# Kernel optimization log

Hardware: AMD Instinct MI355X
Metric: run time of the kernel (lower is better)

## Reference

```python
import jax, jax.numpy as jnp
import numpy as np

EPS = 1e-6

def _layernorm(x, g, b):
    mu = jnp.mean(x, axis=-1, keepdims=True)
    var = jnp.mean(jnp.square(x - mu), axis=-1, keepdims=True)
    return (x - mu) * jax.lax.rsqrt(var + EPS) * g + b

def _mhsa(xq, xk, xv, mask, Wq, bq, Wk, bk, Wv, bv, Wo, bo, num_heads):
    B, Nq, D = xq.shape
    Nk = xk.shape[1]
    dh = D // num_heads
    # project then split heads: [B, N, D] -> [B, H, N, dh]
    def split(x, W, b, N):
        return (x @ W + b).reshape(B, N, num_heads, dh).transpose(0, 2, 1, 3)
    q = split(xq, Wq, bq, Nq)
    k = split(xk, Wk, bk, Nk)
    v = split(xv, Wv, bv, Nk)
    scores = jnp.einsum('bhnd,bhmd->bhnm', q, k) / jnp.sqrt(jnp.float32(dh))
    if mask is not None:
        scores = scores + mask * (-1e9)
    w = jax.nn.softmax(scores, axis=-1)
    out = jnp.einsum('bhnm,bhmd->bhnd', w, v)          # [B,H,Nq,dh]
    out = out.transpose(0, 2, 1, 3).reshape(B, Nq, D)  # concat heads
    return out @ Wo + bo

def setup_inputs() -> dict:
    B, N, D, FF = 2, 2048, 512, 2048
    key = jax.random.key(0)
    ks = jax.random.split(key, 32)
    std = 0.02
    p = {}
    p['inputs'] = jax.random.normal(ks[0], (B, N, D), jnp.float32)
    p['enc_output'] = jax.random.normal(ks[1], (B, N, D), jnp.float32)
    # causal look-ahead mask: 1 where masked (future positions)
    p['look_ahead_mask'] = jnp.triu(jnp.ones((N, N), jnp.float32), k=1)[None, None]
    p['padding_mask'] = jnp.zeros((B, 1, 1, N), jnp.float32)
    i = 2
    for pre in ('q1', 'k1', 'v1', 'o1', 'q2', 'k2', 'v2', 'o2'):
        p[pre + '_w'] = jax.random.normal(ks[i], (D, D), jnp.float32) * std; i += 1
        p[pre + '_b'] = jnp.zeros((D,), jnp.float32)
    p['f1_w'] = jax.random.normal(ks[i], (D, FF), jnp.float32) * std; i += 1
    p['f1_b'] = jnp.zeros((FF,), jnp.float32)
    p['f2_w'] = jax.random.normal(ks[i], (FF, D), jnp.float32) * std; i += 1
    p['f2_b'] = jnp.zeros((D,), jnp.float32)
    for ln in ('ln1', 'ln2', 'ln3'):
        p[ln + '_g'] = jnp.ones((D,), jnp.float32)
        p[ln + '_b'] = jnp.zeros((D,), jnp.float32)
    p['training'] = 0
    return p

def reference(inputs, enc_output, look_ahead_mask, padding_mask,
              q1_w, q1_b, k1_w, k1_b, v1_w, v1_b, o1_w, o1_b,
              q2_w, q2_b, k2_w, k2_b, v2_w, v2_b, o2_w, o2_b,
              f1_w, f1_b, f2_w, f2_b,
              ln1_g, ln1_b, ln2_g, ln2_b, ln3_g, ln3_b,
              training):
    H = 8
    # self-attention (q=k=v=inputs), causal mask; dropout inactive (eval)
    attn1 = _mhsa(inputs, inputs, inputs, look_ahead_mask,
                  q1_w, q1_b, k1_w, k1_b, v1_w, v1_b, o1_w, o1_b, H)
    out1 = _layernorm(inputs + attn1, ln1_g, ln1_b)
    # cross attention: NOTE original arg order -> q=enc, k=enc, v=out1
    attn2 = _mhsa(enc_output, enc_output, out1, padding_mask,
                  q2_w, q2_b, k2_w, k2_b, v2_w, v2_b, o2_w, o2_b, H)
    out2 = _layernorm(out1 + attn2, ln2_g, ln2_b)
    ffn = jax.nn.relu(out2 @ f1_w + f1_b) @ f2_w + f2_b
    return _layernorm(out2 + ffn, ln3_g, ln3_b)
```

## Files before the change

kernel.cpp:

```cpp
#include <hip/hip_runtime.h>

typedef __attribute__((ext_vector_type(8))) _Float16 half8;
typedef __attribute__((ext_vector_type(4))) _Float16 half4;
typedef __attribute__((ext_vector_type(2))) _Float16 half2_t;
typedef __attribute__((ext_vector_type(2))) __fp16 fp16x2;
typedef __attribute__((ext_vector_type(4))) float f32x4;

#define AS1 __attribute__((address_space(1)))
#define AS3 __attribute__((address_space(3)))

constexpr int SEQ = 2048, DM = 512, FFD = 2048, NH = 8, DH = 64;
constexpr int M = 2 * SEQ;
constexpr float QSCALE = 0.125f * 1.4426950408889634f;

__global__ __launch_bounds__(256)
void preproc(const float* __restrict__ q1_w, const float* __restrict__ k1_w,
             const float* __restrict__ v1_w, const float* __restrict__ o1_w,
             const float* __restrict__ q2_w, const float* __restrict__ k2_w,
             const float* __restrict__ v2_w, const float* __restrict__ o2_w,
             const float* __restrict__ f1_w, const float* __restrict__ f2_w,
             _Float16* __restrict__ qk1t, _Float16* __restrict__ v1t,
             _Float16* __restrict__ o1t, _Float16* __restrict__ qk2t,
             _Float16* __restrict__ v2t, _Float16* __restrict__ o2t,
             _Float16* __restrict__ f1t, _Float16* __restrict__ f2t,
             const float* __restrict__ q1_b, const float* __restrict__ k1_b,
             const float* __restrict__ q2_b, const float* __restrict__ k2_b,
             float* __restrict__ qk1b, float* __restrict__ qk2b,
             const float* __restrict__ inp, const float* __restrict__ enc,
             _Float16* __restrict__ xh, _Float16* __restrict__ eh) {
    __shared__ _Float16 tile[64 * 65];
    const int j = blockIdx.x, tid = threadIdx.x;
    if (j < 1024) {
        const float* src; _Float16* dst; int K, N, n0, k0;
        if (j < 512) {
            int w8 = j >> 6, t = j & 63;
            K = 512; N = 512; n0 = (t & 7) * 64; k0 = (t >> 3) * 64;
            switch (w8) {
                case 0: src = q1_w; dst = qk1t; break;
                case 1: src = k1_w; dst = qk1t + 512 * 512; break;
                case 2: src = v1_w; dst = v1t; break;
                case 3: src = o1_w; dst = o1t; break;
                case 4: src = q2_w; dst = qk2t; break;
                case 5: src = k2_w; dst = qk2t + 512 * 512; break;
                case 6: src = v2_w; dst = v2t; break;
                default: src = o2_w; dst = o2t; break;
            }
        } else if (j < 768) {
            int t = j - 512; K = 512; N = 2048;
            n0 = (t % 32) * 64; k0 = (t / 32) * 64; src = f1_w; dst = f1t;
        } else {
            int t = j - 768; K = 2048; N = 512;
            n0 = (t % 8) * 64; k0 = (t / 8) * 64; src = f2_w; dst = f2t;
        }
        int c = tid & 63, r4 = tid >> 6;
        for (int i = 0; i < 16; i++) {
            int r = r4 * 16 + i;
            tile[r * 65 + c] = (_Float16)src[(size_t)(k0 + r) * N + n0 + c];
        }
        __syncthreads();
        for (int i = 0; i < 16; i++) {
            int r = r4 * 16 + i;
            dst[(size_t)(n0 + r) * K + k0 + c] = tile[c * 65 + r];
        }
    } else if (j == 1024) {
        for (int i = tid; i < 512; i += 256) { qk1b[i] = q1_b[i]; qk1b[512 + i] = k1_b[i]; }
    } else if (j == 1025) {
        for (int i = tid; i < 512; i += 256) { qk2b[i] = q2_b[i]; qk2b[512 + i] = k2_b[i]; }
    } else {
        int k = j - 1026;
        const float* s = (k < 1024) ? inp : enc;
        _Float16* d = (k < 1024) ? xh : eh;
        size_t base = (size_t)(k & 1023) * 2048 + tid * 8;
        f32x4 a = *(const f32x4*)(s + base);
        f32x4 b2 = *(const f32x4*)(s + base + 4);
        half8 h;
        h[0] = (_Float16)a[0]; h[1] = (_Float16)a[1];
        h[2] = (_Float16)a[2]; h[3] = (_Float16)a[3];
        h[4] = (_Float16)b2[0]; h[5] = (_Float16)b2[1];
        h[6] = (_Float16)b2[2]; h[7] = (_Float16)b2[3];
        *(half8*)(d + base) = h;
    }
}

__global__ __launch_bounds__(256)
void qkv_gemm(const _Float16* __restrict__ xh, const _Float16* __restrict__ eh,
              const _Float16* __restrict__ qk1t, const _Float16* __restrict__ qk2t,
              const float* __restrict__ qk1b, const float* __restrict__ qk2b,
              _Float16* __restrict__ Qh1, _Float16* __restrict__ Kh1,
              _Float16* __restrict__ Qh2, _Float16* __restrict__ Kh2,
              const _Float16* __restrict__ v1t, const float* __restrict__ v1b,
              _Float16* __restrict__ V1T) {
    __shared__ _Float16 smem[192 * 64];
    const int tid = threadIdx.x;
    const int wid = tid >> 6, lid = tid & 63;
    const int wr = (wid & 1) * 64;
    const int wc = (wid >> 1) * 32;
    const int mi = lid & 15, qd = lid >> 4;
    const int jb = blockIdx.x;
    const _Float16 *Ap, *Bp;
    const float* bias;
    int m0, n0, epi, job = 0;
    if (jb < 1024) {
        epi = 4; job = jb >> 9;
        int L = jb & 511;
        int by = L % 32, bx = L / 32;
        m0 = by * 128; n0 = bx * 64;
        Ap = (job ? eh : xh) + (size_t)m0 * 512;
        Bp = (job ? qk2t : qk1t) + (size_t)n0 * 512;
        bias = job ? qk2b : qk1b;
    } else {
        epi = 3;
        int t = jb - 1024;
        int by = t & 3, bx = t >> 2;
        m0 = by * 128; n0 = bx * 64;
        Ap = v1t + (size_t)m0 * 512;
        Bp = xh + (size_t)n0 * 512;
        bias = v1b;
    }
    const int lrow = lid >> 3;
    const int gblk = (lid & 7) ^ ((lid >> 3) & 7);
    auto stage = [&](int kt) {
        #pragma unroll
        for (int l = 0; l < 4; l++) {
            int c = l * 4 + wid;
            int row = c * 8 + lrow;
            __builtin_amdgcn_global_load_lds(
                (const AS1 unsigned int*)(Ap + (size_t)row * 512 + kt * 64 + gblk * 8),
                (AS3 unsigned int*)&smem[c * 512], 16, 0, 0);
        }
        #pragma unroll
        for (int l = 0; l < 2; l++) {
            int c = l * 4 + wid;
            int row = c * 8 + lrow;
            __builtin_amdgcn_global_load_lds(
                (const AS1 unsigned int*)(Bp + (size_t)row * 512 + kt * 64 + gblk * 8),
                (AS3 unsigned int*)&smem[128 * 64 + c * 512], 16, 0, 0);
        }
    };
    f32x4 acc[4][2] = {};
    stage(0);
    __builtin_amdgcn_s_waitcnt(0x0F70);
    __syncthreads();
    for (int t = 0; t < 8; t++) {
        #pragma unroll
        for (int h = 0; h < 2; h++) {
            const int sA = ((4 * h + qd) ^ (mi & 7)) * 8;
            half8 af[4], bfr[2];
            #pragma unroll
            for (int i = 0; i < 4; i++)
                af[i] = *(const half8*)&smem[(wr + i * 16 + mi) * 64 + sA];
            #pragma unroll
            for (int j = 0; j < 2; j++)
                bfr[j] = *(const half8*)&smem[(128 + wc + j * 16 + mi) * 64 + sA];
            #pragma unroll
            for (int i = 0; i < 4; i++)
                #pragma unroll
                for (int j = 0; j < 2; j++)
                    acc[i][j] = __builtin_amdgcn_mfma_f32_16x16x32_f16(af[i], bfr[j], acc[i][j], 0, 0, 0);
        }
        if (t + 1 < 8) {
            __syncthreads();
            stage(t + 1);
            __builtin_amdgcn_s_waitcnt(0x0F70);
            __syncthreads();
        }
    }
    #pragma unroll
    for (int i = 0; i < 4; i++) {
        #pragma unroll
        for (int j = 0; j < 2; j++) {
            #pragma unroll
            for (int r = 0; r < 4; r++) {
                int row = m0 + wr + i * 16 + qd * 4 + r;
                int col = n0 + wc + j * 16 + mi;
                float v = acc[i][j][r];
                if (epi == 4) {
                    v += bias[col];
                    int hh2 = (col >> 6) & 7, d = col & 63;
                    int bb = row >> 11, nn = row & 2047;
                    size_t idx = (((size_t)bb * 8 + hh2) * SEQ + nn) * 64 + d;
                    if (col < 512) (job ? Qh2 : Qh1)[idx] = (_Float16)(v * QSCALE);
                    else           (job ? Kh2 : Kh1)[idx] = (_Float16)v;
                } else {
                    v += bias[row];
                    V1T[(size_t)row * 4096 + col] = (_Float16)v;
                }
            }
        }
    }
}

template<int BM, int BN, int WM, int WN, bool RELU, int EPI, int SPLIT>
__global__ __launch_bounds__(256)
void gemm_tn(const _Float16* __restrict__ A, const _Float16* __restrict__ Bt,
             const float* __restrict__ bias,
             float* __restrict__ outF, _Float16* __restrict__ outH,
             int Mtot, int N, int K) {
    constexpr int ROWS = BM + BN;
    __shared__ _Float16 smem[ROWS * 64];
    constexpr int AF = WM / 16, BF = WN / 16;
    constexpr int WROW = BM / WM;
    const int tid = threadIdx.x;
    const int wid = tid >> 6, lid = tid & 63;
    const int wr = (wid % WROW) * WM;
    const int wc = (wid / WROW) * WN;
    const int mi = lid & 15, qd = lid >> 4;
    const int gx = gridDim.x, gy = gridDim.y;
    const int L = blockIdx.y * gx + blockIdx.x;
    const int by = L % gy, bx = L / gy;
    const int m0 = by * BM, n0 = bx * BN;
    const int Kc = K / SPLIT;
    const int kbase = (SPLIT > 1) ? blockIdx.z * Kc : 0;
    const _Float16* Ap = A + (size_t)m0 * K + kbase;
    const _Float16* Bp = Bt + (size_t)n0 * K + kbase;
    const int lrow = lid >> 3;
    const int gblk = (lid & 7) ^ ((lid >> 3) & 7);
    auto stage = [&](int kt) {
        #pragma unroll
        for (int l = 0; l < BM / 32; l++) {
            int c = l * 4 + wid;
            int row = c * 8 + lrow;
            __builtin_amdgcn_global_load_lds(
                (const AS1 unsigned int*)(Ap + (size_t)row * K + kt * 64 + gblk * 8),
                (AS3 unsigned int*)&smem[c * 512], 16, 0, 0);
        }
        #pragma unroll
        for (int l = 0; l < BN / 32; l++) {
            int c = l * 4 + wid;
            int row = c * 8 + lrow;
            __builtin_amdgcn_global_load_lds(
                (const AS1 unsigned int*)(Bp + (size_t)row * K + kt * 64 + gblk * 8),
                (AS3 unsigned int*)&smem[BM * 64 + c * 512], 16, 0, 0);
        }
    };
    f32x4 acc[AF][BF] = {};
    const int NIT = Kc / 64;
    stage(0);
    __builtin_amdgcn_s_waitcnt(0x0F70);
    __syncthreads();
    for (int t = 0; t < NIT; t++) {
        #pragma unroll
        for (int h = 0; h < 2; h++) {
            const int sA = ((4 * h + qd) ^ (mi & 7)) * 8;
            half8 af[AF], bfr[BF];
            #pragma unroll
            for (int i = 0; i < AF; i++)
                af[i] = *(const half8*)&smem[(wr + i * 16 + mi) * 64 + sA];
            #pragma unroll
            for (int j = 0; j < BF; j++)
                bfr[j] = *(const half8*)&smem[(BM + wc + j * 16 + mi) * 64 + sA];
            #pragma unroll
            for (int i = 0; i < AF; i++)
                #pragma unroll
                for (int j = 0; j < BF; j++)
                    acc[i][j] = __builtin_amdgcn_mfma_f32_16x16x32_f16(af[i], bfr[j], acc[i][j], 0, 0, 0);
        }
        if (t + 1 < NIT) {
            __syncthreads();
            stage(t + 1);
            __builtin_amdgcn_s_waitcnt(0x0F70);
            __syncthreads();
        }
    }
    float* oF = outF;
    if (SPLIT > 1 && outF) oF = outF + (size_t)blockIdx.z * Mtot * N;
    _Float16* oH = outH;
    if (EPI == 5) oH = outH + (size_t)blockIdx.z * Mtot * N;
    const bool doBias = bias && (SPLIT == 1 || blockIdx.z == 0);
    #pragma unroll
    for (int i = 0; i < AF; i++) {
        #pragma unroll
        for (int j = 0; j < BF; j++) {
            #pragma unroll
            for (int r = 0; r < 4; r++) {
                int row = m0 + wr + i * 16 + qd * 4 + r;
                int col = n0 + wc + j * 16 + mi;
                float v = acc[i][j][r];
                if (EPI == 3) {
                    v += bias[row];
                    outH[(size_t)row * N + col] = (_Float16)v;
                } else if (EPI == 5) {
                    if (doBias) v += bias[col];
                    oH[(size_t)row * N + col] = (_Float16)v;
                } else {
                    if (doBias) v += bias[col];
                    if (RELU) v = fmaxf(v, 0.f);
                    size_t off = (size_t)row * N + col;
                    if (oF) oF[off] = v;
                    if (outH) outH[off] = (_Float16)v;
                }
            }
        }
    }
}

template<bool CAUSAL>
__global__ __launch_bounds__(512)
void attn_mono(const _Float16* __restrict__ Qh, const _Float16* __restrict__ Kh,
               const _Float16* __restrict__ VT, int ldv,
               _Float16* __restrict__ O) {
    const int x = blockIdx.x, bh = blockIdx.y;
    int qt;
    if (CAUSAL) {
        int half = x >> 1;
        int pick = (x & 1) ^ ((bh >> 3) & 1);
        qt = pick ? half : 31 - half;
    } else {
        qt = x;
    }
    const int nt = CAUSAL ? (qt + 1) : 32;
    const int np = (nt + 1) >> 1;
    __shared__ _Float16 Qs[64 * 64];
    __shared__ _Float16 Ps[2][64 * 64];
    __shared__ _Float16 Ks[2][64 * 64];
    __shared__ _Float16 Vs[2][64 * 64];
    __shared__ float Lsh[64];
    const int tid = threadIdx.x, w = tid >> 6, lane = tid & 63;
    const int w4 = w & 3, st = w >> 2;
    const int mi = lane & 15, qd = lane >> 4;
    const int qbase = qt * 64;
    const int b = bh >> 3, h = bh & 7;
    const _Float16* Qp = Qh + ((size_t)bh * SEQ + qbase) * 64;
    const _Float16* Kp = Kh + (size_t)bh * SEQ * 64;
    const _Float16* Vp = VT + (size_t)(h * 64) * ldv + (size_t)b * SEQ;
    const int lrow = lane >> 3;
    const int gblk = (lane & 7) ^ ((lane >> 3) & 7);
    const int f0 = (qd ^ (mi & 7)) * 8;
    const int f1 = ((qd + 4) ^ (mi & 7)) * 8;

    {
        int r0 = tid >> 3, blk = tid & 7;
        int sw = (blk ^ (r0 & 7)) * 8;
        half8 q0 = *(const half8*)(Qp + r0 * 64 + blk * 8);
        *(half8*)&Qs[r0 * 64 + sw] = q0;
    }
    __syncthreads();
    half8 qb0 = *(half8*)&Qs[(w4 * 16 + mi) * 64 + f0];
    half8 qb1 = *(half8*)&Qs[(w4 * 16 + mi) * 64 + f1];
    f32x4 oacc[4] = {};
    float lacc = 0.f;
    _Float16* Pst = Ps[st];

    for (int i = 0; i < np; i++) {
        const int t = 2 * i + st;
        const bool act = t < nt;
        __syncthreads();
        if (act) {
            #pragma unroll
            for (int l = 0; l < 2; l++) {
                int cc = l * 4 + w4;
                int row = cc * 8 + lrow;
                __builtin_amdgcn_global_load_lds(
                    (const AS1 unsigned int*)(Kp + ((size_t)(t * 64 + row)) * 64 + gblk * 8),
                    (AS3 unsigned int*)&Ks[st][cc * 512], 16, 0, 0);
                __builtin_amdgcn_global_load_lds(
                    (const AS1 unsigned int*)(Vp + (size_t)row * ldv + t * 64 + gblk * 8),
                    (AS3 unsigned int*)&Vs[st][cc * 512], 16, 0, 0);
            }
        }
        __builtin_amdgcn_s_waitcnt(0x0F70);
        __syncthreads();
        if (!act) continue;
        const _Float16* ksb = Ks[st];
        const _Float16* vsb = Vs[st];
        f32x4 s[4];
        #pragma unroll
        for (int j = 0; j < 4; j++) {
            half8 ka0 = *(const half8*)&ksb[(j * 16 + mi) * 64 + f0];
            half8 ka1 = *(const half8*)&ksb[(j * 16 + mi) * 64 + f1];
            f32x4 a = {};
            a = __builtin_amdgcn_mfma_f32_16x16x32_f16(ka0, qb0, a, 0, 0, 0);
            a = __builtin_amdgcn_mfma_f32_16x16x32_f16(ka1, qb1, a, 0, 0, 0);
            s[j] = a;
        }
        if (CAUSAL && t == qt) {
            int qg = qbase + w4 * 16 + mi;
            #pragma unroll
            for (int j = 0; j < 4; j++)
                #pragma unroll
                for (int r = 0; r < 4; r++) {
                    int key = t * 64 + j * 16 + qd * 4 + r;
                    if (key > qg) s[j][r] = -1e30f;
                }
        }
        #pragma unroll
        for (int j = 0; j < 4; j++)
            #pragma unroll
            for (int r = 0; r < 4; r++) {
                float pv = __builtin_amdgcn_exp2f(s[j][r]);
                s[j][r] = pv;
                lacc += pv;
            }
        #pragma unroll
        for (int j = 0; j < 4; j++) {
            fp16x2 lo = __builtin_amdgcn_cvt_pkrtz(s[j][0], s[j][1]);
            fp16x2 hi = __builtin_amdgcn_cvt_pkrtz(s[j][2], s[j][3]);
            half2_t lo2 = __builtin_bit_cast(half2_t, lo);
            half2_t hi2 = __builtin_bit_cast(half2_t, hi);
            half4 pq;
            pq[0] = lo2[0]; pq[1] = lo2[1]; pq[2] = hi2[0]; pq[3] = hi2[1];
            int blkp = (2 * j + (qd >> 1)) ^ (mi & 7);
            *(half4*)&Pst[(w4 * 16 + mi) * 64 + blkp * 8 + (qd & 1) * 4] = pq;
        }
        half8 pa0 = *(half8*)&Pst[(w4 * 16 + mi) * 64 + f0];
        half8 pa1 = *(half8*)&Pst[(w4 * 16 + mi) * 64 + f1];
        #pragma unroll
        for (int j = 0; j < 4; j++) {
            half8 vb0 = *(const half8*)&vsb[(j * 16 + mi) * 64 + f0];
            half8 vb1 = *(const half8*)&vsb[(j * 16 + mi) * 64 + f1];
            oacc[j] = __builtin_amdgcn_mfma_f32_16x16x32_f16(pa0, vb0, oacc[j], 0, 0, 0);
            oacc[j] = __builtin_amdgcn_mfma_f32_16x16x32_f16(pa1, vb1, oacc[j], 0, 0, 0);
        }
    }
    __syncthreads();
    if (st == 1) {
        float* obuf = (float*)Ks;
        float* lbuf = (float*)Vs;
        int base = (w4 * 64 + lane) * 16;
        #pragma unroll
        for (int j = 0; j < 4; j++)
            #pragma unroll
            for (int r = 0; r < 4; r++)
                obuf[base + j * 4 + r] = oacc[j][r];
        lbuf[w4 * 64 + lane] = lacc;
    }
    __syncthreads();
    if (st == 0) {
        const float* obuf = (const float*)Ks;
        const float* lbuf = (const float*)Vs;
        int base = (w4 * 64 + lane) * 16;
        #pragma unroll
        for (int j = 0; j < 4; j++)
            #pragma unroll
            for (int r = 0; r < 4; r++)
                oacc[j][r] += obuf[base + j * 4 + r];
        lacc += lbuf[w4 * 64 + lane];
        lacc += __shfl_xor(lacc, 16, 64);
        lacc += __shfl_xor(lacc, 32, 64);
        if (qd == 0) Lsh[w4 * 16 + mi] = lacc;
    }
    __syncthreads();
    if (st == 0) {
        #pragma unroll
        for (int r = 0; r < 4; r++) {
            float rl = 1.f / Lsh[w4 * 16 + qd * 4 + r];
            int qrow = qbase + w4 * 16 + qd * 4 + r;
            size_t obase = ((size_t)(b * SEQ + qrow)) * 512 + h * 64;
            #pragma unroll
            for (int j = 0; j < 4; j++)
                O[obase + j * 16 + mi] = (_Float16)(oacc[j][r] * rl);
        }
    }
}

template<typename RT>
__global__ __launch_bounds__(256)
void add_ln(const RT* __restrict__ res, const _Float16* __restrict__ y,
            size_t pstride, int nparts,
            const float* __restrict__ g, const float* __restrict__ bb,
            float* __restrict__ outF, _Float16* __restrict__ outH) {
    int row = blockIdx.x;
    int tid = threadIdx.x;
    size_t base = (size_t)row * 512;
    float x0 = (float)res[base + tid];
    float x1 = (float)res[base + tid + 256];
    for (int s = 0; s < nparts; s++) {
        x0 += (float)y[s * pstride + base + tid];
        x1 += (float)y[s * pstride + base + tid + 256];
    }
    float s = x0 + x1, sq = x0 * x0 + x1 * x1;
    #pragma unroll
    for (int off = 32; off > 0; off >>= 1) {
        s += __shfl_xor(s, off, 64);
        sq += __shfl_xor(sq, off, 64);
    }
    __shared__ float ls[4], lq[4];
    int w = tid >> 6;
    if ((tid & 63) == 0) { ls[w] = s; lq[w] = sq; }
    __syncthreads();
    s = ls[0] + ls[1] + ls[2] + ls[3];
    sq = lq[0] + lq[1] + lq[2] + lq[3];
    float mu = s * (1.f / 512.f);
    float var = sq * (1.f / 512.f) - mu * mu;
    float rs = rsqrtf(var + 1e-6f);
    float o0 = (x0 - mu) * rs * g[tid] + bb[tid];
    float o1 = (x1 - mu) * rs * g[tid + 256] + bb[tid + 256];
    if (outF) { outF[base + tid] = o0; outF[base + tid + 256] = o1; }
    if (outH) { outH[base + tid] = (_Float16)o0; outH[base + tid + 256] = (_Float16)o1; }
}

extern "C" void kernel_launch(void* const* d_in, const int* in_sizes, int n_in,
                              void* d_out, int out_size, void* d_ws, size_t ws_size,
                              hipStream_t stream) {
    (void)in_sizes; (void)n_in; (void)out_size; (void)ws_size;
    const float* inp  = (const float*)d_in[0];
    const float* enc  = (const float*)d_in[1];
    const float* q1_w = (const float*)d_in[4];
    const float* q1_b = (const float*)d_in[5];
    const float* k1_w = (const float*)d_in[6];
    const float* k1_b = (const float*)d_in[7];
    const float* v1_w = (const float*)d_in[8];
    const float* v1_b = (const float*)d_in[9];
    const float* o1_w = (const float*)d_in[10];
    const float* o1_b = (const float*)d_in[11];
    const float* q2_w = (const float*)d_in[12];
    const float* q2_b = (const float*)d_in[13];
    const float* k2_w = (const float*)d_in[14];
    const float* k2_b = (const float*)d_in[15];
    const float* v2_w = (const float*)d_in[16];
    const float* v2_b = (const float*)d_in[17];
    const float* o2_w = (const float*)d_in[18];
    const float* o2_b = (const float*)d_in[19];
    const float* f1_w = (const float*)d_in[20];
    const float* f1_b = (const float*)d_in[21];
    const float* f2_w = (const float*)d_in[22];
    const float* f2_b = (const float*)d_in[23];
    const float* ln1_g = (const float*)d_in[24];
    const float* ln1_b = (const float*)d_in[25];
    const float* ln2_g = (const float*)d_in[26];
    const float* ln2_b = (const float*)d_in[27];
    const float* ln3_g = (const float*)d_in[28];
    const float* ln3_b = (const float*)d_in[29];

    char* p = (char*)d_ws;
    auto alloc = [&](size_t bytes) { char* r = p; p += (bytes + 255) & ~(size_t)255; return (void*)r; };
    _Float16* xh    = (_Float16*)alloc((size_t)M * DM * 2);
    _Float16* eh    = (_Float16*)alloc((size_t)M * DM * 2);
    _Float16* qk1t  = (_Float16*)alloc((size_t)1024 * DM * 2);
    _Float16* v1t   = (_Float16*)alloc((size_t)DM * DM * 2);
    _Float16* o1t   = (_Float16*)alloc((size_t)DM * DM * 2);
    _Float16* qk2t  = (_Float16*)alloc((size_t)1024 * DM * 2);
    _Float16* v2t   = (_Float16*)alloc((size_t)DM * DM * 2);
    _Float16* o2t   = (_Float16*)alloc((size_t)DM * DM * 2);
    _Float16* f1t   = (_Float16*)alloc((size_t)FFD * DM * 2);
    _Float16* f2t   = (_Float16*)alloc((size_t)DM * FFD * 2);
    float* qk1b     = (float*)alloc(1024 * 4);
    float* qk2b     = (float*)alloc(1024 * 4);
    _Float16* Qh1   = (_Float16*)alloc((size_t)M * DM * 2);
    _Float16* Kh1   = (_Float16*)alloc((size_t)M * DM * 2);
    _Float16* Qh2   = (_Float16*)alloc((size_t)M * DM * 2);
    _Float16* Kh2   = (_Float16*)alloc((size_t)M * DM * 2);
    _Float16* V1T   = (_Float16*)alloc((size_t)DM * M * 2);
    _Float16* V2T   = (_Float16*)alloc((size_t)DM * M * 2);
    _Float16* Ah    = (_Float16*)alloc((size_t)M * DM * 2);
    _Float16* Ph    = (_Float16*)alloc((size_t)2 * M * DM * 2);
    _Float16* out1h = (_Float16*)alloc((size_t)M * DM * 2);
    _Float16* out2h = (_Float16*)alloc((size_t)M * DM * 2);
    _Float16* hh    = (_Float16*)alloc((size_t)M * FFD * 2);
    const size_t PS = (size_t)M * DM;

    dim3 t256(256), t512(512);
    preproc<<<dim3(1026 + 2048), t256, 0, stream>>>(
        q1_w, k1_w, v1_w, o1_w, q2_w, k2_w, v2_w, o2_w, f1_w, f2_w,
        qk1t, v1t, o1t, qk2t, v2t, o2t, f1t, f2t,
        q1_b, k1_b, q2_b, k2_b, qk1b, qk2b, inp, enc, xh, eh);

    qkv_gemm<<<dim3(1280), t256, 0, stream>>>(
        xh, eh, qk1t, qk2t, qk1b, qk2b, Qh1, Kh1, Qh2, Kh2, v1t, v1_b, V1T);

    attn_mono<true><<<dim3(32, 16), t512, 0, stream>>>(Qh1, Kh1, V1T, M, Ah);
    gemm_tn<64, 64, 32, 32, false, 5, 2><<<dim3(8, 64, 2), t256, 0, stream>>>(
        Ah, o1t, o1_b, nullptr, Ph, M, 512, 512);
    add_ln<float><<<dim3(M), t256, 0, stream>>>(inp, Ph, PS, 2, ln1_g, ln1_b, nullptr, out1h);

    gemm_tn<64, 64, 32, 32, false, 3, 1><<<dim3(64, 8), t256, 0, stream>>>(
        v2t, out1h, v2_b, nullptr, V2T, 512, M, 512);
    attn_mono<false><<<dim3(32, 16), t512, 0, stream>>>(Qh2, Kh2, V2T, M, Ah);
    gemm_tn<64, 64, 32, 32, false, 5, 2><<<dim3(8, 64, 2), t256, 0, stream>>>(
        Ah, o2t, o2_b, nullptr, Ph, M, 512, 512);
    add_ln<_Float16><<<dim3(M), t256, 0, stream>>>(out1h, Ph, PS, 2, ln2_g, ln2_b, nullptr, out2h);

    gemm_tn<128, 64, 64, 32, true, 0, 1><<<dim3(32, 32), t256, 0, stream>>>(
        out2h, f1t, f1_b, nullptr, hh, M, 2048, 512);
    gemm_tn<64, 64, 32, 32, false, 5, 2><<<dim3(8, 64, 2), t256, 0, stream>>>(
        hh, f2t, f2_b, nullptr, Ph, M, 512, 2048);
    add_ln<_Float16><<<dim3(M), t256, 0, stream>>>(out2h, Ph, PS, 2, ln3_g, ln3_b, (float*)d_out, nullptr);
}
```

Baseline: 304.9 us.

## Fuse attention output projection with residual add and layernorm

Adds a kernel in which each 512-thread block computes a full 64x512 row tile of the output projection, then applies bias, the residual add and layernorm in registers using cross-wave reductions through shared memory. It replaces the split-K GEMM plus separate add_ln launch for both attention blocks, removing the fp16 partial-sum round-trip and one launch each. The cost is far less parallelism: only 64 blocks on a many-CU GPU, each looping serially over K with a non-double-buffered load/sync pattern.

```diff
diff --git a/kernel.cpp b/kernel.cpp
--- a/kernel.cpp
+++ b/kernel.cpp
@@ -294,6 +294,128 @@
     }
 }
 
+template<typename RT>
+__global__ __launch_bounds__(512)
+void oproj_ln(const _Float16* __restrict__ A, const _Float16* __restrict__ Bt,
+              const float* __restrict__ bias, const RT* __restrict__ res,
+              const float* __restrict__ lng, const float* __restrict__ lnb,
+              _Float16* __restrict__ outH) {
+    __shared__ _Float16 smem[576 * 64];
+    __shared__ float sred[8][64], qred[8][64];
+    const int tid = threadIdx.x;
+    const int wid = tid >> 6, lid = tid & 63;
+    const int mi = lid & 15, qd = lid >> 4;
+    const int m0 = blockIdx.x * 64;
+    const int wc = wid * 64;
+    const _Float16* Ap = A + (size_t)m0 * 512;
+    const int lrow = lid >> 3;
+    const int gblk = (lid & 7) ^ ((lid >> 3) & 7);
+    auto stage = [&](int kt) {
+        {
+            int c = wid;
+            int row = c * 8 + lrow;
+            __builtin_amdgcn_global_load_lds(
+                (const AS1 unsigned int*)(Ap + (size_t)row * 512 + kt * 64 + gblk * 8),
+                (AS3 unsigned int*)&smem[c * 512], 16, 0, 0);
+        }
+        #pragma unroll
+        for (int l = 0; l < 8; l++) {
+            int c = l * 8 + wid;
+            int row = c * 8 + lrow;
+            __builtin_amdgcn_global_load_lds(
+                (const AS1 unsigned int*)(Bt + (size_t)row * 512 + kt * 64 + gblk * 8),
+                (AS3 unsigned int*)&smem[(8 + c) * 512], 16, 0, 0);
+        }
+    };
+    f32x4 acc[4][4] = {};
+    stage(0);
+    __builtin_amdgcn_s_waitcnt(0x0F70);
+    __syncthreads();
+    for (int t = 0; t < 8; t++) {
+        #pragma unroll
+        for (int h = 0; h < 2; h++) {
+            const int sA = ((4 * h + qd) ^ (mi & 7)) * 8;
+            half8 af[4], bfr[4];
+            #pragma unroll
+            for (int i = 0; i < 4; i++)
+                af[i] = *(const half8*)&smem[(i * 16 + mi) * 64 + sA];
+            #pragma unroll
+            for (int j = 0; j < 4; j++)
+                bfr[j] = *(const half8*)&smem[(64 + wc + j * 16 + mi) * 64 + sA];
+            #pragma unroll
+            for (int i = 0; i < 4; i++)
+                #pragma unroll
+                for (int j = 0; j < 4; j++)
+                    acc[i][j] = __builtin_amdgcn_mfma_f32_16x16x32_f16(af[i], bfr[j], acc[i][j], 0, 0, 0);
+        }
+        if (t + 1 < 8) {
+            __syncthreads();
+            stage(t + 1);
+            __builtin_amdgcn_s_waitcnt(0x0F70);
+            __syncthreads();
+        }
+    }
+    float ps[4][4], pq[4][4];
+    #pragma unroll
+    for (int i = 0; i < 4; i++)
+        #pragma unroll
+        for (int r = 0; r < 4; r++) { ps[i][r] = 0.f; pq[i][r] = 0.f; }
+    #pragma unroll
+    for (int i = 0; i < 4; i++)
+        #pragma unroll
+        for (int j = 0; j < 4; j++) {
+            int col = wc + j * 16 + mi;
+            float bj = bias[col];
+            #pragma unroll
+            for (int r = 0; r < 4; r++) {
+                int row = m0 + i * 16 + qd * 4 + r;
+                float x = acc[i][j][r] + bj + (float)res[(size_t)row * 512 + col];
+                acc[i][j][r] = x;
+                ps[i][r] += x; pq[i][r] += x * x;
+            }
+        }
+    #pragma unroll
+    for (int i = 0; i < 4; i++)
+        #pragma unroll
+        for (int r = 0; r < 4; r++) {
+            float s = ps[i][r], q = pq[i][r];
+            s += __shfl_xor(s, 1, 64); q += __shfl_xor(q, 1, 64);
+            s += __shfl_xor(s, 2, 64); q += __shfl_xor(q, 2, 64);
+            s += __shfl_xor(s, 4, 64); q += __shfl_xor(q, 4, 64);
+            s += __shfl_xor(s, 8, 64); q += __shfl_xor(q, 8, 64);
+            ps[i][r] = s; pq[i][r] = q;
+        }
+    if (mi == 0) {
+        #pragma unroll
+        for (int i = 0; i < 4; i++)
+            #pragma unroll
+            for (int r = 0; r < 4; r++) {
+                sred[wid][i * 16 + qd * 4 + r] = ps[i][r];
+                qred[wid][i * 16 + qd * 4 + r] = pq[i][r];
+            }
+    }
+    __syncthreads();
+    #pragma unroll
+    for (int i = 0; i < 4; i++)
+        #pragma unroll
+        for (int r = 0; r < 4; r++) {
+            int lr = i * 16 + qd * 4 + r;
+            float ts = 0.f, tq = 0.f;
+            #pragma unroll
+            for (int w2 = 0; w2 < 8; w2++) { ts += sred[w2][lr]; tq += qred[w2][lr]; }
+            float mu = ts * (1.f / 512.f);
+            float var = tq * (1.f / 512.f) - mu * mu;
+            float rs = rsqrtf(var + 1e-6f);
+            int row = m0 + lr;
+            #pragma unroll
+            for (int j = 0; j < 4; j++) {
+                int col = wc + j * 16 + mi;
+                float o = (acc[i][j][r] - mu) * rs * lng[col] + lnb[col];
+                outH[(size_t)row * 512 + col] = (_Float16)o;
+            }
+        }
+}
+
 template<bool CAUSAL>
 __global__ __launch_bounds__(512)
 void attn_mono(const _Float16* __restrict__ Qh, const _Float16* __restrict__ Kh,
@@ -559,16 +681,14 @@
         xh, eh, qk1t, qk2t, qk1b, qk2b, Qh1, Kh1, Qh2, Kh2, v1t, v1_b, V1T);
 
     attn_mono<true><<<dim3(32, 16), t512, 0, stream>>>(Qh1, Kh1, V1T, M, Ah);
-    gemm_tn<64, 64, 32, 32, false, 5, 2><<<dim3(8, 64, 2), t256, 0, stream>>>(
-        Ah, o1t, o1_b, nullptr, Ph, M, 512, 512);
-    add_ln<float><<<dim3(M), t256, 0, stream>>>(inp, Ph, PS, 2, ln1_g, ln1_b, nullptr, out1h);
+    oproj_ln<float><<<dim3(64), t512, 0, stream>>>(
+        Ah, o1t, o1_b, inp, ln1_g, ln1_b, out1h);
 
     gemm_tn<64, 64, 32, 32, false, 3, 1><<<dim3(64, 8), t256, 0, stream>>>(
         v2t, out1h, v2_b, nullptr, V2T, 512, M, 512);
     attn_mono<false><<<dim3(32, 16), t512, 0, stream>>>(Qh2, Kh2, V2T, M, Ah);
-    gemm_tn<64, 64, 32, 32, false, 5, 2><<<dim3(8, 64, 2), t256, 0, stream>>>(
-        Ah, o2t, o2_b, nullptr, Ph, M, 512, 512);
-    add_ln<_Float16><<<dim3(M), t256, 0, stream>>>(out1h, Ph, PS, 2, ln2_g, ln2_b, nullptr, out2h);
+    oproj_ln<_Float16><<<dim3(64), t512, 0, stream>>>(
+        Ah, o2t, o2_b, out1h, ln2_g, ln2_b, out2h);
 
     gemm_tn<128, 64, 64, 32, true, 0, 1><<<dim3(32, 32), t256, 0, stream>>>(
         out2h, f1t, f1_b, nullptr, hh, M, 2048, 512);
```

New measurement: 316.0 us. 1.04x slower.
